# Kernel optimization log

Measured on AMD Instinct MI355X. Metric: run time of the kernel, lower is better.

## Reference

```python
import jax, jax.numpy as jnp
import numpy as np

V, E, L, H, B, T = 32000, 1024, 6, 16, 4, 1024
HS = E // H
FF = 4 * E


def setup_inputs() -> dict:
    key = jax.random.key(0)
    ks = jax.random.split(key, 16)
    s = 0.02
    n = lambda k, shp: jax.random.normal(k, shp, jnp.float32) * s
    return {
        "tokens": jax.random.randint(ks[0], (B, T), 0, V),
        "tok_emb": n(ks[1], (V, E)),
        "pos_emb": n(ks[2], (T, E)),
        "Wq": n(ks[3], (L, E, E)),
        "Wk": n(ks[4], (L, E, E)),
        "Wv": n(ks[5], (L, E, E)),
        "Wo": n(ks[6], (L, E, E)),
        "ln1_g": jnp.ones((L, E), jnp.float32),
        "ln1_b": jnp.zeros((L, E), jnp.float32),
        "W1": n(ks[7], (L, E, FF)),
        "b1": jnp.zeros((L, FF), jnp.float32),
        "W2": n(ks[8], (L, FF, E)),
        "b2": jnp.zeros((L, E), jnp.float32),
        "ln2_g": jnp.ones((L, E), jnp.float32),
        "ln2_b": jnp.zeros((L, E), jnp.float32),
        "lmh_w": n(ks[9], (E, V)),
        "lmh_b": jnp.zeros((V,), jnp.float32),
    }


def _layernorm(x, g, b):
    m = jnp.mean(x, axis=-1, keepdims=True)
    v = jnp.var(x, axis=-1, keepdims=True)
    return (x - m) * jax.lax.rsqrt(v + 1e-5) * g + b


def _forward(tokens, tok_emb, pos_emb, Wq, Wk, Wv, Wo, ln1_g, ln1_b,
             W1, b1, W2, b2, ln2_g, ln2_b, lmh_w, lmh_b):
    Bb, Tt = tokens.shape
    x = tok_emb[tokens] + pos_emb[:Tt]  # [B,T,E]
    mask = jnp.tril(jnp.ones((Tt, Tt), bool))  # causal
    scale = jnp.float32(E) ** -0.5  # NOTE: original scales by emb_dim, not head_size

    def block(x, p):
        wq, wk, wv, wo, g1, be1, w1, bb1, w2, bb2, g2, be2 = p
        h = _layernorm(x, g1, be1)
        q = (h @ wq).reshape(Bb, Tt, H, HS)
        k = (h @ wk).reshape(Bb, Tt, H, HS)
        v = (h @ wv).reshape(Bb, Tt, H, HS)
        scores = jnp.einsum('bqhd,bkhd->bhqk', q, k) * scale
        scores = jnp.where(mask, scores, -jnp.inf)
        w = jax.nn.softmax(scores, axis=-1)
        attn = jnp.einsum('bhqk,bkhd->bqhd', w, v).reshape(Bb, Tt, E)
        x = x + attn @ wo
        h2 = _layernorm(x, g2, be2)
        x = x + jax.nn.relu(h2 @ w1 + bb1) @ w2 + bb2
        return x, None

    x, _ = jax.lax.scan(block, x, (Wq, Wk, Wv, Wo, ln1_g, ln1_b,
                                   W1, b1, W2, b2, ln2_g, ln2_b))
    logits = x @ lmh_w + lmh_b  # [B,T,V]
    return logits


def reference(tokens, tok_emb, pos_emb, Wq, Wk, Wv, Wo, ln1_g, ln1_b,
              W1, b1, W2, b2, ln2_g, ln2_b, lmh_w, lmh_b):
    return _forward(tokens, tok_emb, pos_emb, Wq, Wk, Wv, Wo, ln1_g, ln1_b,
                    W1, b1, W2, b2, ln2_g, ln2_b, lmh_w, lmh_b)
```

## Files before the change

kernel.cpp:

```cpp
#include <hip/hip_runtime.h>
#include <cstdint>
#include <cstddef>

typedef __bf16 bf16;
typedef __attribute__((ext_vector_type(8))) __bf16 bf16x8;
typedef __attribute__((ext_vector_type(4))) float f32x4;

constexpr int kV = 32000, kE = 1024, kL = 6, kH = 16, kB = 4, kT = 1024;
constexpr int kHS = 64, kFF = 4096;
constexpr int kM = kB * kT;
constexpr float kScale = 0.03125f;

typedef __attribute__((address_space(1))) void gv_t;
typedef __attribute__((address_space(3))) void lv_t;

__device__ inline void gload_lds16(const void* g, void* l) {
  __builtin_amdgcn_global_load_lds((gv_t*)g, (lv_t*)l, 16, 0, 0);
}

enum { EPI_BF16 = 0, EPI_BF16_BIAS_RELU = 1, EPI_F32 = 2, EPI_F32_RES = 3, EPI_F32_BIAS = 4 };

template <int EPI>
__global__ __launch_bounds__(512, 2) void gemm256_k(
    const bf16* __restrict__ Ag, const bf16* __restrict__ Bg, void* Cg,
    const float* __restrict__ bias, const float* __restrict__ resid,
    int K, long lda, long ldb, long ldc) {
  extern __shared__ bf16 lds[];
  constexpr int SL = 8192;
  bf16* As = lds;
  bf16* Bs = lds + 4 * SL;

  const int tid = threadIdx.x, lane = tid & 63, w = tid >> 6;
  int bx = blockIdx.x, by = blockIdx.y;
  {
    int gx = gridDim.x, gy = gridDim.y;
    int nxy = gx * gy;
    int orig = by * gx + bx;
    int q = nxy >> 3, r = nxy & 7, xcd = orig & 7, idx = orig >> 3;
    int logical = (xcd < r ? xcd * (q + 1) : r * (q + 1) + (xcd - r) * q) + idx;
    bx = logical / gy;
    by = logical % gy;
  }
  const long tm = (long)by * 256, tn = (long)bx * 256;
  const int wr = w >> 2, wc = w & 3;
  const int lr = lane & 15, kg = lane >> 4;

  const int p0 = tid, p1 = 512 + tid;
  const int r0 = p0 >> 2, ls0 = (p0 & 3) ^ ((r0 >> 1) & 3);
  const int r1 = p1 >> 2, ls1 = (p1 & 3) ^ ((r1 >> 1) & 3);
  const bf16* a0 = Ag + (tm + r0) * lda + ls0 * 8;
  const bf16* a1 = Ag + (tm + r1) * lda + ls1 * 8;
  const bf16* b0 = Bg + (tn + r0) * ldb + ls0 * 8;
  const bf16* b1 = Bg + (tn + r1) * ldb + ls1 * 8;
  const int wb = w * 1024;

  auto stage = [&](int s) {
    const int slot = s & 3;
    const long k0 = (long)s * 32;
    char* Ab = (char*)As + slot * (SL * 2);
    char* Bb = (char*)Bs + slot * (SL * 2);
    gload_lds16(a0 + k0, Ab + wb);
    gload_lds16(a1 + k0, Ab + 8192 + wb);
    gload_lds16(b0 + k0, Bb + wb);
    gload_lds16(b1 + k0, Bb + 8192 + wb);
  };

  int aoff[8], boff[4];
#pragma unroll
  for (int mi = 0; mi < 8; mi++) {
    int ar = wr * 128 + mi * 16 + lr;
    aoff[mi] = ar * 64 + ((kg ^ ((ar >> 1) & 3)) << 4);
  }
#pragma unroll
  for (int ni = 0; ni < 4; ni++) {
    int br = wc * 64 + ni * 16 + lr;
    boff[ni] = br * 64 + ((kg ^ ((br >> 1) & 3)) << 4);
  }

  f32x4 acc[8][4] = {};
  stage(0);
  stage(1);
  stage(2);
  const int NS = K >> 5;
  for (int s = 0; s < NS; s++) {
    __builtin_amdgcn_sched_barrier(0);
    if (s <= NS - 3)
      asm volatile("s_waitcnt vmcnt(8)" ::: "memory");
    else if (s == NS - 2)
      asm volatile("s_waitcnt vmcnt(4)" ::: "memory");
    else
      asm volatile("s_waitcnt vmcnt(0)" ::: "memory");
    __builtin_amdgcn_s_barrier();
    __builtin_amdgcn_sched_barrier(0);
    if (s + 3 < NS) stage(s + 3);
    const char* Ab = (const char*)As + (s & 3) * (SL * 2);
    const char* Bb = (const char*)Bs + (s & 3) * (SL * 2);
    bf16x8 af[8], bfr[4];
#pragma unroll
    for (int mi = 0; mi < 8; mi++) af[mi] = *(const bf16x8*)(Ab + aoff[mi]);
#pragma unroll
    for (int ni = 0; ni < 4; ni++) bfr[ni] = *(const bf16x8*)(Bb + boff[ni]);
    __builtin_amdgcn_s_setprio(1);
#pragma unroll
    for (int mi = 0; mi < 8; mi++)
#pragma unroll
      for (int ni = 0; ni < 4; ni++)
        acc[mi][ni] =
            __builtin_amdgcn_mfma_f32_16x16x32_bf16(af[mi], bfr[ni], acc[mi][ni], 0, 0, 0);
    __builtin_amdgcn_s_setprio(0);
  }

#pragma unroll
  for (int mi = 0; mi < 8; mi++) {
#pragma unroll
    for (int ni = 0; ni < 4; ni++) {
      const long rr = tm + wr * 128 + mi * 16 + kg * 4;
      const long cc = tn + wc * 64 + ni * 16 + lr;
      float bi = 0.f;
      if constexpr (EPI == EPI_BF16_BIAS_RELU || EPI == EPI_F32_BIAS) bi = bias[cc];
      if constexpr (EPI == EPI_F32_RES) bi = bias ? bias[cc] : 0.f;
#pragma unroll
      for (int j = 0; j < 4; j++) {
        long off = (rr + j) * ldc + cc;
        float val = acc[mi][ni][j];
        if constexpr (EPI == EPI_BF16)
          ((bf16*)Cg)[off] = (bf16)val;
        else if constexpr (EPI == EPI_BF16_BIAS_RELU)
          ((bf16*)Cg)[off] = (bf16)fmaxf(val + bi, 0.f);
        else if constexpr (EPI == EPI_F32)
          ((float*)Cg)[off] = val;
        else if constexpr (EPI == EPI_F32_RES)
          ((float*)Cg)[off] = resid[off] + val + bi;
        else
          ((float*)Cg)[off] = val + bi;
      }
    }
  }
}

template <int BM, int BN, int WM, int WN, int EPI, bool CAUSAL>
__global__ __launch_bounds__((BM / WM) * (BN / WN) * 64) void gemm_k(
    const bf16* __restrict__ Ag, const bf16* __restrict__ Bg, void* Cg,
    const float* __restrict__ bias, const float* resid, int K, long lda, long ldb,
    long ldc, long sA1, long sA2, long sB1, long sB2, long sC1, long sC2, int zdiv) {
  constexpr int BK = 32;
  constexpr int NWM = BM / WM, NWN = BN / WN, NW = NWM * NWN, THREADS = NW * 64;
  constexpr int MI = WM / 16, NI = WN / 16;
  constexpr int A_CH = (BM * BK * 2) / (THREADS * 16);
  constexpr int B_CH = (BN * BK * 2) / (THREADS * 16);
  static_assert(A_CH >= 1 && B_CH >= 1, "staging chunks");
  __shared__ bf16 As[2][BM * BK];
  __shared__ bf16 Bs[2][BN * BK];
  const int tid = threadIdx.x, lane = tid & 63;
  int bx = blockIdx.x, by = blockIdx.y;
  const int z = blockIdx.z;
  if (gridDim.z == 1) {
    int gx = gridDim.x, gy = gridDim.y;
    int nxy = gx * gy;
    int orig = by * gx + bx;
    int q = nxy >> 3, r = nxy & 7, xcd = orig & 7, idx = orig >> 3;
    int logical = (xcd < r ? xcd * (q + 1) : r * (q + 1) + (xcd - r) * q) + idx;
    bx = logical / gy;
    by = logical % gy;
  }
  const long tm = (long)by * BM, tn = (long)bx * BN;
  if (CAUSAL && tn > tm + (BM - 1)) return;
  const int zq = z / zdiv, zr = z % zdiv;
  Ag += (long)zq * sA1 + (long)zr * sA2;
  Bg += (long)zq * sB1 + (long)zr * sB2;
  const long cbase = (long)zq * sC1 + (long)zr * sC2;
  const int w = tid >> 6;
  const int wr = w / NWN, wc = w % NWN;
  const int wm0 = wr * WM, wn0 = wc * WN;
  const int lr = lane & 15, kg = lane >> 4;
  f32x4 acc[MI][NI] = {};

  auto stage = [&](int buf, int k0) {
#pragma unroll
    for (int i = 0; i < A_CH; i++) {
      int qq = i * THREADS + tid;
      gload_lds16(Ag + (tm + (qq >> 2)) * lda + k0 + (qq & 3) * 8,
                  (char*)&As[buf][0] + (i * THREADS + (tid & ~63)) * 16);
    }
#pragma unroll
    for (int i = 0; i < B_CH; i++) {
      int qq = i * THREADS + tid;
      gload_lds16(Bg + (tn + (qq >> 2)) * ldb + k0 + (qq & 3) * 8,
                  (char*)&Bs[buf][0] + (i * THREADS + (tid & ~63)) * 16);
    }
  };

  const int nt = K / BK;
  stage(0, 0);
  __syncthreads();
  int cur = 0;
  for (int t = 0; t < nt; t++) {
    if (t + 1 < nt) stage(cur ^ 1, (t + 1) * BK);
    bf16x8 af[MI], bfr[NI];
#pragma unroll
    for (int mi = 0; mi < MI; mi++)
      af[mi] = *(const bf16x8*)&As[cur][(wm0 + mi * 16 + lr) * BK + kg * 8];
#pragma unroll
    for (int ni = 0; ni < NI; ni++)
      bfr[ni] = *(const bf16x8*)&Bs[cur][(wn0 + ni * 16 + lr) * BK + kg * 8];
#pragma unroll
    for (int mi = 0; mi < MI; mi++)
#pragma unroll
      for (int ni = 0; ni < NI; ni++)
        acc[mi][ni] =
            __builtin_amdgcn_mfma_f32_16x16x32_bf16(af[mi], bfr[ni], acc[mi][ni], 0, 0, 0);
    __syncthreads();
    cur ^= 1;
  }

#pragma unroll
  for (int mi = 0; mi < MI; mi++) {
#pragma unroll
    for (int ni = 0; ni < NI; ni++) {
      const long rr = tm + wm0 + mi * 16 + kg * 4;
      const long cc = tn + wn0 + ni * 16 + lr;
      float bi = 0.f;
      if constexpr (EPI == EPI_BF16_BIAS_RELU || EPI == EPI_F32_BIAS) bi = bias[cc];
      if constexpr (EPI == EPI_F32_RES) bi = bias ? bias[cc] : 0.f;
#pragma unroll
      for (int j = 0; j < 4; j++) {
        long off = cbase + (rr + j) * ldc + cc;
        float val = acc[mi][ni][j];
        if constexpr (EPI == EPI_BF16)
          ((bf16*)Cg)[off] = (bf16)val;
        else if constexpr (EPI == EPI_BF16_BIAS_RELU)
          ((bf16*)Cg)[off] = (bf16)fmaxf(val + bi, 0.f);
        else if constexpr (EPI == EPI_F32)
          ((float*)Cg)[off] = val;
        else if constexpr (EPI == EPI_F32_RES)
          ((float*)Cg)[off] = resid[off] + val + bi;
        else
          ((float*)Cg)[off] = val + bi;
      }
    }
  }
}

__global__ __launch_bounds__(256, 2) void fa_k(const bf16* __restrict__ qkv,
                                               bf16* __restrict__ out) {
  extern __shared__ bf16 lds[];
  char* L = (char*)lds;
  const int tid = threadIdx.x, lane = tid & 63, wq = tid >> 6;
  const int lr = lane & 15, kg = lane >> 4;
  const int bt = blockIdx.x, z = blockIdx.y;
  const int b = z >> 4, hh = z & 15;
  const long bq = (long)b * kT;
  const int q0 = bt * 128;
  const bf16* qbase = qkv + (bq + q0) * 3072 + hh * 64;

#pragma unroll
  for (int i = 0; i < 4; i++) {
    int p = i * 256 + tid;
    int row = p >> 3, s = p & 7;
    gload_lds16(qbase + (long)row * 3072 + ((s ^ (row & 7)) * 8),
                L + (i * 256 + (tid & ~63)) * 16);
  }
  auto stageKV = [&](int buf, int t) {
    const bf16* kb = qkv + (bq + t * 64) * 3072 + 1024 + hh * 64;
#pragma unroll
    for (int i = 0; i < 2; i++) {
      int p = i * 256 + tid;
      int key = p >> 3, s = p & 7;
      gload_lds16(kb + (long)key * 3072 + ((s ^ (key & 7)) * 8),
                  L + 16384 + buf * 8192 + (i * 256 + (tid & ~63)) * 16);
      gload_lds16(kb + (long)key * 3072 + 1024 + s * 8,
                  L + 32768 + buf * 8192 + (i * 256 + (tid & ~63)) * 16);
    }
  };
  stageKV(0, 0);
  __syncthreads();

  bf16x8 qf[2][2];
#pragma unroll
  for (int mi = 0; mi < 2; mi++)
#pragma unroll
    for (int ks = 0; ks < 2; ks++) {
      int qr = wq * 32 + mi * 16 + lr;
      qf[mi][ks] = *(const bf16x8*)(L + qr * 128 + ((ks * 64 + kg * 16) ^ ((qr & 7) << 4)));
    }

  f32x4 O[2][4] = {};
  float mrun[2][4], lrun[2][4];
#pragma unroll
  for (int mi = 0; mi < 2; mi++)
#pragma unroll
    for (int j = 0; j < 4; j++) {
      mrun[mi][j] = -3e38f;
      lrun[mi][j] = 0.f;
    }
  char* Pw = L + 58368 + wq * 4608;

  const int nt = 2 * bt + 2;
  int cur = 0;
  for (int t = 0; t < nt; t++) {
    if (t + 1 < nt) stageKV(cur ^ 1, t + 1);
    {
      const char* Vb = L + 32768 + cur * 8192;
      char* VTb = L + 49152;
#pragma unroll
      for (int i = 0; i < 2; i++) {
        int p = i * 256 + tid;
        int key = p >> 3, s = p & 7;
        bf16x8 vv = *(const bf16x8*)(Vb + p * 16);
#pragma unroll
        for (int e = 0; e < 8; e++)
          *(bf16*)(VTb + (s * 8 + e) * 144 + ((key * 2) ^ (s << 4))) = vv[e];
      }
    }
    asm volatile("s_waitcnt lgkmcnt(0)" ::: "memory");
    __builtin_amdgcn_sched_barrier(0);
    __builtin_amdgcn_s_barrier();
    __builtin_amdgcn_sched_barrier(0);

    const char* Kb = L + 16384 + cur * 8192;
    f32x4 S[2][4] = {};
#pragma unroll
    for (int ks = 0; ks < 2; ks++) {
      bf16x8 kf[4];
#pragma unroll
      for (int ni = 0; ni < 4; ni++) {
        int key = ni * 16 + lr;
        kf[ni] = *(const bf16x8*)(Kb + key * 128 + ((ks * 64 + kg * 16) ^ ((key & 7) << 4)));
      }
#pragma unroll
      for (int mi = 0; mi < 2; mi++)
#pragma unroll
        for (int ni = 0; ni < 4; ni++)
          S[mi][ni] = __builtin_amdgcn_mfma_f32_16x16x32_bf16(qf[mi][ks], kf[ni], S[mi][ni], 0, 0, 0);
    }

    const int kv0 = t * 64;
#pragma unroll
    for (int mi = 0; mi < 2; mi++) {
      const int qg = q0 + wq * 32 + mi * 16 + kg * 4;
#pragma unroll
      for (int j = 0; j < 4; j++) {
        float m0 = -3e38f;
#pragma unroll
        for (int ni = 0; ni < 4; ni++) {
          float v = (kv0 + ni * 16 + lr > qg + j) ? -3e38f : S[mi][ni][j];
          S[mi][ni][j] = v;
          m0 = fmaxf(m0, v);
        }
        m0 = fmaxf(m0, __shfl_xor(m0, 1));
        m0 = fmaxf(m0, __shfl_xor(m0, 2));
        m0 = fmaxf(m0, __shfl_xor(m0, 4));
        m0 = fmaxf(m0, __shfl_xor(m0, 8));
        float mnew = fmaxf(mrun[mi][j], m0);
        float alpha = __expf((mrun[mi][j] - mnew) * kScale);
        mrun[mi][j] = mnew;
        lrun[mi][j] *= alpha;
#pragma unroll
        for (int di = 0; di < 4; di++) O[mi][di][j] *= alpha;
        float rs = 0.f;
#pragma unroll
        for (int ni = 0; ni < 4; ni++) {
          float v = S[mi][ni][j];
          float p = (v <= -1e38f) ? 0.f : __expf((v - mnew) * kScale);
          S[mi][ni][j] = p;
          rs += p;
        }
        rs += __shfl_xor(rs, 1);
        rs += __shfl_xor(rs, 2);
        rs += __shfl_xor(rs, 4);
        rs += __shfl_xor(rs, 8);
        lrun[mi][j] += rs;
      }
#pragma unroll
      for (int ni = 0; ni < 4; ni++)
#pragma unroll
        for (int j = 0; j < 4; j++)
          *(bf16*)(Pw + (mi * 16 + kg * 4 + j) * 144 + (ni * 16 + lr) * 2) =
              (bf16)S[mi][ni][j];
    }
    asm volatile("s_waitcnt lgkmcnt(0)" ::: "memory");
    __builtin_amdgcn_sched_barrier(0);

    const char* VTb = L + 49152;
#pragma unroll
    for (int ks = 0; ks < 2; ks++) {
      bf16x8 pf[2], vf[4];
#pragma unroll
      for (int mi = 0; mi < 2; mi++)
        pf[mi] = *(const bf16x8*)(Pw + (mi * 16 + lr) * 144 + ks * 64 + kg * 16);
#pragma unroll
      for (int di = 0; di < 4; di++) {
        int d = di * 16 + lr;
        vf[di] = *(const bf16x8*)(VTb + d * 144 + ((ks * 64 + kg * 16) ^ (((d >> 3) & 7) << 4)));
      }
#pragma unroll
      for (int mi = 0; mi < 2; mi++)
#pragma unroll
        for (int di = 0; di < 4; di++)
          O[mi][di] = __builtin_amdgcn_mfma_f32_16x16x32_bf16(pf[mi], vf[di], O[mi][di], 0, 0, 0);
    }
    __syncthreads();
    cur ^= 1;
  }

#pragma unroll
  for (int mi = 0; mi < 2; mi++)
#pragma unroll
    for (int j = 0; j < 4; j++) {
      float inv = 1.f / lrun[mi][j];
      long grow = bq + q0 + wq * 32 + mi * 16 + kg * 4 + j;
#pragma unroll
      for (int di = 0; di < 4; di++)
        out[grow * kE + hh * 64 + di * 16 + lr] = (bf16)(O[mi][di][j] * inv);
    }
}

__global__ void tcvt_k(const float* __restrict__ in, bf16* __restrict__ out, int K, int N,
                       long in_zs, long out_zs) {
  __shared__ float t[32][33];
  long z = blockIdx.z;
  in += z * in_zs;
  out += z * out_zs;
  int n0 = blockIdx.x * 32, k0 = blockIdx.y * 32;
  int tx = threadIdx.x, ty = threadIdx.y;
#pragma unroll
  for (int i = 0; i < 32; i += 8) t[ty + i][tx] = in[(long)(k0 + ty + i) * N + n0 + tx];
  __syncthreads();
#pragma unroll
  for (int i = 0; i < 32; i += 8)
    out[(long)(n0 + ty + i) * K + k0 + tx] = (bf16)t[tx][ty + i];
}

__global__ void embed_k(const int* __restrict__ toks, const float* __restrict__ te,
                        const float* __restrict__ pe, float* __restrict__ x) {
  int row = blockIdx.x, tid = threadIdx.x;
  int t = row & (kT - 1);
  long tok = toks[row];
  float4 a = ((const float4*)(te + tok * kE))[tid];
  float4 p = ((const float4*)(pe + (long)t * kE))[tid];
  float4 r{a.x + p.x, a.y + p.y, a.z + p.z, a.w + p.w};
  ((float4*)(x + (long)row * kE))[tid] = r;
}

__global__ void ln_k(const float* __restrict__ x, const float* __restrict__ g,
                     const float* __restrict__ b, bf16* __restrict__ h) {
  int row = blockIdx.x, tid = threadIdx.x, lane = tid & 63, w = tid >> 6;
  const float4 v = ((const float4*)(x + (long)row * kE))[tid];
  float s = v.x + v.y + v.z + v.w;
  float ss = v.x * v.x + v.y * v.y + v.z * v.z + v.w * v.w;
#pragma unroll
  for (int o = 32; o; o >>= 1) {
    s += __shfl_xor(s, o);
    ss += __shfl_xor(ss, o);
  }
  __shared__ float r1[4], r2[4];
  if (lane == 0) { r1[w] = s; r2[w] = ss; }
  __syncthreads();
  s = r1[0] + r1[1] + r1[2] + r1[3];
  ss = r2[0] + r2[1] + r2[2] + r2[3];
  float mean = s * (1.f / kE);
  float var = ss * (1.f / kE) - mean * mean;
  float rs = rsqrtf(var + 1e-5f);
  float4 gg = ((const float4*)g)[tid];
  float4 bb = ((const float4*)b)[tid];
  union { bf16 o[4]; uint2 u; } pk;
  pk.o[0] = (bf16)((v.x - mean) * rs * gg.x + bb.x);
  pk.o[1] = (bf16)((v.y - mean) * rs * gg.y + bb.y);
  pk.o[2] = (bf16)((v.z - mean) * rs * gg.z + bb.z);
  pk.o[3] = (bf16)((v.w - mean) * rs * gg.w + bb.w);
  ((uint2*)(h + (long)row * kE))[tid] = pk.u;
}

__global__ void cast_k(const float* __restrict__ x, bf16* __restrict__ o) {
  long i = (long)blockIdx.x * 256 + threadIdx.x;
  float4 v = ((const float4*)x)[i];
  union { bf16 b[4]; uint2 u; } pk;
  pk.b[0] = (bf16)v.x;
  pk.b[1] = (bf16)v.y;
  pk.b[2] = (bf16)v.z;
  pk.b[3] = (bf16)v.w;
  ((uint2*)o)[i] = pk.u;
}

extern "C" void kernel_launch(void* const* d_in, const int* in_sizes, int n_in,
                              void* d_out, int out_size, void* d_ws, size_t ws_size,
                              hipStream_t stream) {
  const int* toks = (const int*)d_in[0];
  const float* te = (const float*)d_in[1];
  const float* pe = (const float*)d_in[2];
  const float* Wq = (const float*)d_in[3];
  const float* Wk = (const float*)d_in[4];
  const float* Wv = (const float*)d_in[5];
  const float* Wo = (const float*)d_in[6];
  const float* g1 = (const float*)d_in[7];
  const float* be1 = (const float*)d_in[8];
  const float* W1 = (const float*)d_in[9];
  const float* bb1 = (const float*)d_in[10];
  const float* W2 = (const float*)d_in[11];
  const float* bb2 = (const float*)d_in[12];
  const float* g2 = (const float*)d_in[13];
  const float* be2 = (const float*)d_in[14];
  const float* lmw = (const float*)d_in[15];
  const float* lmb = (const float*)d_in[16];

  hipFuncSetAttribute(reinterpret_cast<const void*>(&gemm256_k<EPI_BF16>),
                      hipFuncAttributeMaxDynamicSharedMemorySize, 131072);
  hipFuncSetAttribute(reinterpret_cast<const void*>(&gemm256_k<EPI_BF16_BIAS_RELU>),
                      hipFuncAttributeMaxDynamicSharedMemorySize, 131072);
  hipFuncSetAttribute(reinterpret_cast<const void*>(&gemm256_k<EPI_F32_BIAS>),
                      hipFuncAttributeMaxDynamicSharedMemorySize, 131072);
  hipFuncSetAttribute(reinterpret_cast<const void*>(&fa_k),
                      hipFuncAttributeMaxDynamicSharedMemorySize, 76800);

  char* ws = (char*)d_ws;
  size_t off = 0;
  auto alloc = [&](size_t bytes) -> char* {
    char* p = ws + off;
    off += (bytes + 255) & ~(size_t)255;
    return p;
  };
  bf16* WqkvT = (bf16*)alloc((size_t)kL * 3 * kE * kE * 2);
  bf16* WoT = (bf16*)alloc((size_t)kL * kE * kE * 2);
  bf16* W1T = (bf16*)alloc((size_t)kL * kE * kFF * 2);
  bf16* W2T = (bf16*)alloc((size_t)kL * kE * kFF * 2);
  bf16* lmT = (bf16*)alloc((size_t)kV * kE * 2);
  float* x = (float*)alloc((size_t)kM * kE * 4);
  bf16* h = (bf16*)alloc((size_t)kM * kE * 2);
  bf16* qkv = (bf16*)alloc((size_t)kM * 3 * kE * 2);
  bf16* at = (bf16*)alloc((size_t)kM * kE * 2);

  bf16* mid = (bf16*)d_out;

  const long EE = (long)kE * kE;
  dim3 tb(32, 8);
  tcvt_k<<<dim3(kE / 32, kE / 32, kL), tb, 0, stream>>>(Wq, WqkvT, kE, kE, EE, 3 * EE);
  tcvt_k<<<dim3(kE / 32, kE / 32, kL), tb, 0, stream>>>(Wk, WqkvT + EE, kE, kE, EE, 3 * EE);
  tcvt_k<<<dim3(kE / 32, kE / 32, kL), tb, 0, stream>>>(Wv, WqkvT + 2 * EE, kE, kE, EE, 3 * EE);
  tcvt_k<<<dim3(kE / 32, kE / 32, kL), tb, 0, stream>>>(Wo, WoT, kE, kE, EE, EE);
  tcvt_k<<<dim3(kFF / 32, kE / 32, kL), tb, 0, stream>>>(W1, W1T, kE, kFF, 4 * EE, 4 * EE);
  tcvt_k<<<dim3(kE / 32, kFF / 32, kL), tb, 0, stream>>>(W2, W2T, kFF, kE, 4 * EE, 4 * EE);
  tcvt_k<<<dim3(kV / 32, kE / 32, 1), tb, 0, stream>>>(lmw, lmT, kE, kV, 0, 0);

  embed_k<<<kM, 256, 0, stream>>>(toks, te, pe, x);

  for (int l = 0; l < kL; l++) {
    ln_k<<<kM, 256, 0, stream>>>(x, g1 + l * kE, be1 + l * kE, h);
    gemm256_k<EPI_BF16><<<dim3(3 * kE / 256, kM / 256), 512, 131072, stream>>>(
        h, WqkvT + (size_t)l * 3 * EE, qkv, nullptr, nullptr, kE, kE, kE, 3 * kE);
    fa_k<<<dim3(kT / 128, kB * kH), 256, 76800, stream>>>(qkv, at);
    gemm_k<128, 128, 64, 64, EPI_F32_RES, false><<<dim3(kE / 128, kM / 128, 1), 256, 0, stream>>>(
        at, WoT + (size_t)l * EE, x, nullptr, x, kE, kE, kE, kE, 0, 0, 0, 0, 0, 0, 1);
    ln_k<<<kM, 256, 0, stream>>>(x, g2 + l * kE, be2 + l * kE, h);
    gemm256_k<EPI_BF16_BIAS_RELU><<<dim3(kFF / 256, kM / 256), 512, 131072, stream>>>(
        h, W1T + (size_t)l * (size_t)kFF * kE, mid, bb1 + l * kFF, nullptr, kE, kE, kE, kFF);
    gemm_k<128, 128, 64, 64, EPI_F32_RES, false><<<dim3(kE / 128, kM / 128, 1), 256, 0, stream>>>(
        mid, W2T + (size_t)l * (size_t)kE * kFF, x, bb2 + l * kE, x, kFF, kFF, kFF, kE, 0, 0, 0,
        0, 0, 0, 1);
  }
  cast_k<<<kM * kE / 1024, 256, 0, stream>>>(x, h);
  gemm256_k<EPI_F32_BIAS><<<dim3(kV / 256, kM / 256), 512, 131072, stream>>>(
      h, lmT, d_out, lmb, nullptr, kE, kE, kE, kV);
}
```

Baseline: 2.428 ms.

## Restructure GEMM main loop into double-buffered 64-K ping-pong phases

Replaces the 4-slot, 32-K-per-stage software pipeline in the 256x256 GEMM with two 64KB buffers of 64-K tiles. Each tile is split into four quarter phases that interleave LDS fragment reads, staging of the next tile's quarter, and MFMA blocks, separated by workgroup barriers. The goal is finer overlap of global->LDS copies with MFMA and better hiding of LDS read latency. The cost is many more s_barriers per iteration and a shallower prefetch distance, which could stall waves. The attention kernel edits only swap inline asm for macros.

```diff
diff --git a/kernel.cpp b/kernel.cpp
--- a/kernel.cpp
+++ b/kernel.cpp
@@ -17,6 +17,11 @@
 __device__ inline void gload_lds16(const void* g, void* l) {
   __builtin_amdgcn_global_load_lds((gv_t*)g, (lv_t*)l, 16, 0, 0);
 }
+
+#define SB0() __builtin_amdgcn_sched_barrier(0)
+#define LGK0() asm volatile("s_waitcnt lgkmcnt(0)" ::: "memory")
+#define VM4() asm volatile("s_waitcnt vmcnt(4)" ::: "memory")
+#define VM0() asm volatile("s_waitcnt vmcnt(0)" ::: "memory")
 
 enum { EPI_BF16 = 0, EPI_BF16_BIAS_RELU = 1, EPI_F32 = 2, EPI_F32_RES = 3, EPI_F32_BIAS = 4 };
 
@@ -26,9 +31,7 @@
     const float* __restrict__ bias, const float* __restrict__ resid,
     int K, long lda, long ldb, long ldc) {
   extern __shared__ bf16 lds[];
-  constexpr int SL = 8192;
-  bf16* As = lds;
-  bf16* Bs = lds + 4 * SL;
+  char* Lb = (char*)lds;
 
   const int tid = threadIdx.x, lane = tid & 63, w = tid >> 6;
   int bx = blockIdx.x, by = blockIdx.y;
@@ -45,24 +48,20 @@
   const int wr = w >> 2, wc = w & 3;
   const int lr = lane & 15, kg = lane >> 4;
 
-  const int p0 = tid, p1 = 512 + tid;
-  const int r0 = p0 >> 2, ls0 = (p0 & 3) ^ ((r0 >> 1) & 3);
-  const int r1 = p1 >> 2, ls1 = (p1 & 3) ^ ((r1 >> 1) & 3);
-  const bf16* a0 = Ag + (tm + r0) * lda + ls0 * 8;
-  const bf16* a1 = Ag + (tm + r1) * lda + ls1 * 8;
-  const bf16* b0 = Bg + (tn + r0) * ldb + ls0 * 8;
-  const bf16* b1 = Bg + (tn + r1) * ldb + ls1 * 8;
-  const int wb = w * 1024;
-
-  auto stage = [&](int s) {
-    const int slot = s & 3;
-    const long k0 = (long)s * 32;
-    char* Ab = (char*)As + slot * (SL * 2);
-    char* Bb = (char*)Bs + slot * (SL * 2);
-    gload_lds16(a0 + k0, Ab + wb);
-    gload_lds16(a1 + k0, Ab + 8192 + wb);
-    gload_lds16(b0 + k0, Bb + wb);
-    gload_lds16(b1 + k0, Bb + 8192 + wb);
+  const int r0 = tid >> 2, g0 = (tid & 3) ^ ((r0 >> 1) & 3);
+  const int r1 = (512 + tid) >> 2, g1 = ((512 + tid) & 3) ^ ((r1 >> 1) & 3);
+  const bf16* a0 = Ag + (tm + r0) * lda + g0 * 8;
+  const bf16* a1 = Ag + (tm + r1) * lda + g1 * 8;
+  const bf16* b0 = Bg + (tn + r0) * ldb + g0 * 8;
+  const bf16* b1 = Bg + (tn + r1) * ldb + g1 * 8;
+  const int wdst = (tid & ~63) * 16;
+
+  auto stageH = [&](int buf, int which, long k0) {
+    char* dst = Lb + buf * 65536 + which * 16384;
+    const bf16* s0 = (which < 2) ? a0 : b0;
+    const bf16* s1 = (which < 2) ? a1 : b1;
+    gload_lds16(s0 + k0, dst + wdst);
+    gload_lds16(s1 + k0, dst + 8192 + wdst);
   };
 
   int aoff[8], boff[4];
@@ -78,36 +77,92 @@
   }
 
   f32x4 acc[8][4] = {};
-  stage(0);
-  stage(1);
-  stage(2);
-  const int NS = K >> 5;
-  for (int s = 0; s < NS; s++) {
-    __builtin_amdgcn_sched_barrier(0);
-    if (s <= NS - 3)
-      asm volatile("s_waitcnt vmcnt(8)" ::: "memory");
-    else if (s == NS - 2)
-      asm volatile("s_waitcnt vmcnt(4)" ::: "memory");
-    else
-      asm volatile("s_waitcnt vmcnt(0)" ::: "memory");
-    __builtin_amdgcn_s_barrier();
-    __builtin_amdgcn_sched_barrier(0);
-    if (s + 3 < NS) stage(s + 3);
-    const char* Ab = (const char*)As + (s & 3) * (SL * 2);
-    const char* Bb = (const char*)Bs + (s & 3) * (SL * 2);
-    bf16x8 af[8], bfr[4];
-#pragma unroll
-    for (int mi = 0; mi < 8; mi++) af[mi] = *(const bf16x8*)(Ab + aoff[mi]);
-#pragma unroll
-    for (int ni = 0; ni < 4; ni++) bfr[ni] = *(const bf16x8*)(Bb + boff[ni]);
+  stageH(0, 0, 0);
+  stageH(0, 2, 0);
+  stageH(0, 1, 32);
+  stageH(0, 3, 32);
+  VM4();
+  __syncthreads();
+
+  const int NT = K >> 6;
+  bf16x8 fa[4], fb[4], fa2[4];
+  for (int t = 0; t < NT; t++) {
+    const char* base = Lb + (t & 1) * 65536;
+    const int nb = (t + 1) & 1;
+    const bool pf = (t + 1 < NT);
+    const long kn = (long)(t + 1) * 64;
+#pragma unroll
+    for (int mi = 0; mi < 4; mi++) fa[mi] = *(const bf16x8*)(base + aoff[mi]);
+#pragma unroll
+    for (int ni = 0; ni < 4; ni++) fb[ni] = *(const bf16x8*)(base + 32768 + boff[ni]);
+    if (pf) stageH(nb, 0, kn);
+    SB0();
+    __builtin_amdgcn_s_barrier();
+    LGK0();
+    SB0();
     __builtin_amdgcn_s_setprio(1);
 #pragma unroll
-    for (int mi = 0; mi < 8; mi++)
+    for (int mi = 0; mi < 4; mi++)
 #pragma unroll
       for (int ni = 0; ni < 4; ni++)
-        acc[mi][ni] =
-            __builtin_amdgcn_mfma_f32_16x16x32_bf16(af[mi], bfr[ni], acc[mi][ni], 0, 0, 0);
+        acc[mi][ni] = __builtin_amdgcn_mfma_f32_16x16x32_bf16(fa[mi], fb[ni], acc[mi][ni], 0, 0, 0);
     __builtin_amdgcn_s_setprio(0);
+    SB0();
+    __builtin_amdgcn_s_barrier();
+#pragma unroll
+    for (int mi = 0; mi < 4; mi++) fa2[mi] = *(const bf16x8*)(base + aoff[4 + mi]);
+    if (pf) stageH(nb, 2, kn);
+    if (pf) VM4(); else VM0();
+    SB0();
+    __builtin_amdgcn_s_barrier();
+    LGK0();
+    SB0();
+    __builtin_amdgcn_s_setprio(1);
+#pragma unroll
+    for (int mi = 0; mi < 4; mi++)
+#pragma unroll
+      for (int ni = 0; ni < 4; ni++)
+        acc[4 + mi][ni] =
+            __builtin_amdgcn_mfma_f32_16x16x32_bf16(fa2[mi], fb[ni], acc[4 + mi][ni], 0, 0, 0);
+    __builtin_amdgcn_s_setprio(0);
+    SB0();
+    __builtin_amdgcn_s_barrier();
+#pragma unroll
+    for (int mi = 0; mi < 4; mi++) fa[mi] = *(const bf16x8*)(base + 16384 + aoff[mi]);
+#pragma unroll
+    for (int ni = 0; ni < 4; ni++) fb[ni] = *(const bf16x8*)(base + 49152 + boff[ni]);
+    if (pf) stageH(nb, 1, kn + 32);
+    SB0();
+    __builtin_amdgcn_s_barrier();
+    LGK0();
+    SB0();
+    __builtin_amdgcn_s_setprio(1);
+#pragma unroll
+    for (int mi = 0; mi < 4; mi++)
+#pragma unroll
+      for (int ni = 0; ni < 4; ni++)
+        acc[mi][ni] = __builtin_amdgcn_mfma_f32_16x16x32_bf16(fa[mi], fb[ni], acc[mi][ni], 0, 0, 0);
+    __builtin_amdgcn_s_setprio(0);
+    SB0();
+    __builtin_amdgcn_s_barrier();
+#pragma unroll
+    for (int mi = 0; mi < 4; mi++) fa2[mi] = *(const bf16x8*)(base + 16384 + aoff[4 + mi]);
+    if (pf) stageH(nb, 3, kn + 32);
+    if (pf) VM4();
+    SB0();
+    __builtin_amdgcn_s_barrier();
+    LGK0();
+    SB0();
+    __builtin_amdgcn_s_setprio(1);
+#pragma unroll
+    for (int mi = 0; mi < 4; mi++)
+#pragma unroll
+      for (int ni = 0; ni < 4; ni++)
+        acc[4 + mi][ni] =
+            __builtin_amdgcn_mfma_f32_16x16x32_bf16(fa2[mi], fb[ni], acc[4 + mi][ni], 0, 0, 0);
+    __builtin_amdgcn_s_setprio(0);
+    SB0();
+    __builtin_amdgcn_s_barrier();
   }
 
 #pragma unroll
@@ -312,10 +367,10 @@
           *(bf16*)(VTb + (s * 8 + e) * 144 + ((key * 2) ^ (s << 4))) = vv[e];
       }
     }
-    asm volatile("s_waitcnt lgkmcnt(0)" ::: "memory");
-    __builtin_amdgcn_sched_barrier(0);
-    __builtin_amdgcn_s_barrier();
-    __builtin_amdgcn_sched_barrier(0);
+    LGK0();
+    SB0();
+    __builtin_amdgcn_s_barrier();
+    SB0();
 
     const char* Kb = L + 16384 + cur * 8192;
     f32x4 S[2][4] = {};
@@ -378,8 +433,8 @@
           *(bf16*)(Pw + (mi * 16 + kg * 4 + j) * 144 + (ni * 16 + lr) * 2) =
               (bf16)S[mi][ni][j];
     }
-    asm volatile("s_waitcnt lgkmcnt(0)" ::: "memory");
-    __builtin_amdgcn_sched_barrier(0);
+    LGK0();
+    SB0();
 
     const char* VTb = L + 49152;
 #pragma unroll
```

After: 2.436 ms. About the same (+0.3%).

## Pair causal attention query tiles per block and use ring-buffered 128-tile W2 GEMM

Applied to the files above, without the earlier changes.

The flash-attention kernel now processes two query tiles per block (tile p and 7-p), so every block does the same amount of causal work and the grid shrinks to four blocks per head. The FFN down-projection GEMM moves to a new 128x128 kernel with a 4-slot global_load_lds ring buffer and deeper prefetch, replacing the 2-buffer generic GEMM. Both changes aim to reduce tail imbalance and memory-latency stalls. In exchange, the attention launch has fewer blocks, and the new GEMM uses 64KB of LDS, which may limit occupancy.

```diff
diff --git a/kernel.cpp b/kernel.cpp
--- a/kernel.cpp
+++ b/kernel.cpp
@@ -18,7 +18,20 @@
   __builtin_amdgcn_global_load_lds((gv_t*)g, (lv_t*)l, 16, 0, 0);
 }
 
+#define SB0() __builtin_amdgcn_sched_barrier(0)
+#define LGK0() asm volatile("s_waitcnt lgkmcnt(0)" ::: "memory")
+
 enum { EPI_BF16 = 0, EPI_BF16_BIAS_RELU = 1, EPI_F32 = 2, EPI_F32_RES = 3, EPI_F32_BIAS = 4 };
+
+__device__ inline void xcd_swz(int& bx, int& by) {
+  int gx = gridDim.x, gy = gridDim.y;
+  int nxy = gx * gy;
+  int orig = by * gx + bx;
+  int q = nxy >> 3, r = nxy & 7, xcd = orig & 7, idx = orig >> 3;
+  int logical = (xcd < r ? xcd * (q + 1) : r * (q + 1) + (xcd - r) * q) + idx;
+  bx = logical / gy;
+  by = logical % gy;
+}
 
 template <int EPI>
 __global__ __launch_bounds__(512, 2) void gemm256_k(
@@ -32,15 +45,7 @@
 
   const int tid = threadIdx.x, lane = tid & 63, w = tid >> 6;
   int bx = blockIdx.x, by = blockIdx.y;
-  {
-    int gx = gridDim.x, gy = gridDim.y;
-    int nxy = gx * gy;
-    int orig = by * gx + bx;
-    int q = nxy >> 3, r = nxy & 7, xcd = orig & 7, idx = orig >> 3;
-    int logical = (xcd < r ? xcd * (q + 1) : r * (q + 1) + (xcd - r) * q) + idx;
-    bx = logical / gy;
-    by = logical % gy;
-  }
+  xcd_swz(bx, by);
   const long tm = (long)by * 256, tn = (long)bx * 256;
   const int wr = w >> 2, wc = w & 3;
   const int lr = lane & 15, kg = lane >> 4;
@@ -83,7 +88,7 @@
   stage(2);
   const int NS = K >> 5;
   for (int s = 0; s < NS; s++) {
-    __builtin_amdgcn_sched_barrier(0);
+    SB0();
     if (s <= NS - 3)
       asm volatile("s_waitcnt vmcnt(8)" ::: "memory");
     else if (s == NS - 2)
@@ -91,7 +96,7 @@
     else
       asm volatile("s_waitcnt vmcnt(0)" ::: "memory");
     __builtin_amdgcn_s_barrier();
-    __builtin_amdgcn_sched_barrier(0);
+    SB0();
     if (s + 3 < NS) stage(s + 3);
     const char* Ab = (const char*)As + (s & 3) * (SL * 2);
     const char* Bb = (const char*)Bs + (s & 3) * (SL * 2);
@@ -115,6 +120,112 @@
 #pragma unroll
     for (int ni = 0; ni < 4; ni++) {
       const long rr = tm + wr * 128 + mi * 16 + kg * 4;
+      const long cc = tn + wc * 64 + ni * 16 + lr;
+      float bi = 0.f;
+      if constexpr (EPI == EPI_BF16_BIAS_RELU || EPI == EPI_F32_BIAS) bi = bias[cc];
+      if constexpr (EPI == EPI_F32_RES) bi = bias ? bias[cc] : 0.f;
+#pragma unroll
+      for (int j = 0; j < 4; j++) {
+        long off = (rr + j) * ldc + cc;
+        float val = acc[mi][ni][j];
+        if constexpr (EPI == EPI_BF16)
+          ((bf16*)Cg)[off] = (bf16)val;
+        else if constexpr (EPI == EPI_BF16_BIAS_RELU)
+          ((bf16*)Cg)[off] = (bf16)fmaxf(val + bi, 0.f);
+        else if constexpr (EPI == EPI_F32)
+          ((float*)Cg)[off] = val;
+        else if constexpr (EPI == EPI_F32_RES)
+          ((float*)Cg)[off] = resid[off] + val + bi;
+        else
+          ((float*)Cg)[off] = val + bi;
+      }
+    }
+  }
+}
+
+template <int EPI>
+__global__ __launch_bounds__(256, 2) void ring128_k(
+    const bf16* __restrict__ Ag, const bf16* __restrict__ Bg, void* Cg,
+    const float* __restrict__ bias, const float* __restrict__ resid,
+    int K, long lda, long ldb, long ldc) {
+  extern __shared__ bf16 lds[];
+  char* Lb = (char*)lds;
+  const int tid = threadIdx.x, lane = tid & 63, w = tid >> 6;
+  int bx = blockIdx.x, by = blockIdx.y;
+  xcd_swz(bx, by);
+  const long tm = (long)by * 128, tn = (long)bx * 128;
+  const int wr = w >> 1, wc = w & 1;
+  const int lr = lane & 15, kg = lane >> 4;
+
+  const int r0 = tid >> 2, g0 = (tid & 3) ^ ((r0 >> 1) & 3);
+  const int r1 = (256 + tid) >> 2, g1 = ((256 + tid) & 3) ^ ((r1 >> 1) & 3);
+  const bf16* a0 = Ag + (tm + r0) * lda + g0 * 8;
+  const bf16* a1 = Ag + (tm + r1) * lda + g1 * 8;
+  const bf16* b0 = Bg + (tn + r0) * ldb + g0 * 8;
+  const bf16* b1 = Bg + (tn + r1) * ldb + g1 * 8;
+  const int wb = w * 1024;
+
+  auto stage = [&](int s) {
+    const int slot = s & 3;
+    const long k0 = (long)s * 32;
+    char* Ab = Lb + slot * 16384;
+    char* Bb = Ab + 8192;
+    gload_lds16(a0 + k0, Ab + wb);
+    gload_lds16(a1 + k0, Ab + 4096 + wb);
+    gload_lds16(b0 + k0, Bb + wb);
+    gload_lds16(b1 + k0, Bb + 4096 + wb);
+  };
+
+  int aoff[4], boff[4];
+#pragma unroll
+  for (int mi = 0; mi < 4; mi++) {
+    int ar = wr * 64 + mi * 16 + lr;
+    aoff[mi] = ar * 64 + ((kg ^ ((ar >> 1) & 3)) << 4);
+  }
+#pragma unroll
+  for (int ni = 0; ni < 4; ni++) {
+    int br = wc * 64 + ni * 16 + lr;
+    boff[ni] = br * 64 + ((kg ^ ((br >> 1) & 3)) << 4);
+  }
+
+  f32x4 acc[4][4] = {};
+  stage(0);
+  stage(1);
+  stage(2);
+  const int NS = K >> 5;
+  for (int s = 0; s < NS; s++) {
+    SB0();
+    if (s <= NS - 3)
+      asm volatile("s_waitcnt vmcnt(8)" ::: "memory");
+    else if (s == NS - 2)
+      asm volatile("s_waitcnt vmcnt(4)" ::: "memory");
+    else
+      asm volatile("s_waitcnt vmcnt(0)" ::: "memory");
+    __builtin_amdgcn_s_barrier();
+    SB0();
+    if (s + 3 < NS) stage(s + 3);
+    const char* Ab = Lb + (s & 3) * 16384;
+    const char* Bb = Ab + 8192;
+    bf16x8 af[4], bfr[4];
+#pragma unroll
+    for (int mi = 0; mi < 4; mi++) af[mi] = *(const bf16x8*)(Ab + aoff[mi]);
+#pragma unroll
+    for (int ni = 0; ni < 4; ni++) bfr[ni] = *(const bf16x8*)(Bb + boff[ni]);
+    __builtin_amdgcn_s_setprio(1);
+#pragma unroll
+    for (int mi = 0; mi < 4; mi++)
+#pragma unroll
+      for (int ni = 0; ni < 4; ni++)
+        acc[mi][ni] =
+            __builtin_amdgcn_mfma_f32_16x16x32_bf16(af[mi], bfr[ni], acc[mi][ni], 0, 0, 0);
+    __builtin_amdgcn_s_setprio(0);
+  }
+
+#pragma unroll
+  for (int mi = 0; mi < 4; mi++) {
+#pragma unroll
+    for (int ni = 0; ni < 4; ni++) {
+      const long rr = tm + wr * 64 + mi * 16 + kg * 4;
       const long cc = tn + wc * 64 + ni * 16 + lr;
       float bi = 0.f;
       if constexpr (EPI == EPI_BF16_BIAS_RELU || EPI == EPI_F32_BIAS) bi = bias[cc];
@@ -154,15 +265,7 @@
   const int tid = threadIdx.x, lane = tid & 63;
   int bx = blockIdx.x, by = blockIdx.y;
   const int z = blockIdx.z;
-  if (gridDim.z == 1) {
-    int gx = gridDim.x, gy = gridDim.y;
-    int nxy = gx * gy;
-    int orig = by * gx + bx;
-    int q = nxy >> 3, r = nxy & 7, xcd = orig & 7, idx = orig >> 3;
-    int logical = (xcd < r ? xcd * (q + 1) : r * (q + 1) + (xcd - r) * q) + idx;
-    bx = logical / gy;
-    by = logical % gy;
-  }
+  if (gridDim.z == 1) xcd_swz(bx, by);
   const long tm = (long)by * BM, tn = (long)bx * BN;
   if (CAUSAL && tn > tm + (BM - 1)) return;
   const int zq = z / zdiv, zr = z % zdiv;
@@ -247,19 +350,10 @@
   char* L = (char*)lds;
   const int tid = threadIdx.x, lane = tid & 63, wq = tid >> 6;
   const int lr = lane & 15, kg = lane >> 4;
-  const int bt = blockIdx.x, z = blockIdx.y;
+  const int pair = blockIdx.x, z = blockIdx.y;
   const int b = z >> 4, hh = z & 15;
   const long bq = (long)b * kT;
-  const int q0 = bt * 128;
-  const bf16* qbase = qkv + (bq + q0) * 3072 + hh * 64;
-
-#pragma unroll
-  for (int i = 0; i < 4; i++) {
-    int p = i * 256 + tid;
-    int row = p >> 3, s = p & 7;
-    gload_lds16(qbase + (long)row * 3072 + ((s ^ (row & 7)) * 8),
-                L + (i * 256 + (tid & ~63)) * 16);
-  }
+
   auto stageKV = [&](int buf, int t) {
     const bf16* kb = qkv + (bq + t * 64) * 3072 + 1024 + hh * 64;
 #pragma unroll
@@ -272,147 +366,164 @@
                   L + 32768 + buf * 8192 + (i * 256 + (tid & ~63)) * 16);
     }
   };
-  stageKV(0, 0);
-  __syncthreads();
-
-  bf16x8 qf[2][2];
-#pragma unroll
-  for (int mi = 0; mi < 2; mi++)
-#pragma unroll
-    for (int ks = 0; ks < 2; ks++) {
-      int qr = wq * 32 + mi * 16 + lr;
-      qf[mi][ks] = *(const bf16x8*)(L + qr * 128 + ((ks * 64 + kg * 16) ^ ((qr & 7) << 4)));
-    }
-
-  f32x4 O[2][4] = {};
-  float mrun[2][4], lrun[2][4];
-#pragma unroll
-  for (int mi = 0; mi < 2; mi++)
-#pragma unroll
-    for (int j = 0; j < 4; j++) {
-      mrun[mi][j] = -3e38f;
-      lrun[mi][j] = 0.f;
-    }
   char* Pw = L + 58368 + wq * 4608;
 
-  const int nt = 2 * bt + 2;
-  int cur = 0;
-  for (int t = 0; t < nt; t++) {
-    if (t + 1 < nt) stageKV(cur ^ 1, t + 1);
-    {
-      const char* Vb = L + 32768 + cur * 8192;
-      char* VTb = L + 49152;
-#pragma unroll
-      for (int i = 0; i < 2; i++) {
-        int p = i * 256 + tid;
-        int key = p >> 3, s = p & 7;
-        bf16x8 vv = *(const bf16x8*)(Vb + p * 16);
-#pragma unroll
-        for (int e = 0; e < 8; e++)
-          *(bf16*)(VTb + (s * 8 + e) * 144 + ((key * 2) ^ (s << 4))) = vv[e];
-      }
-    }
-    asm volatile("s_waitcnt lgkmcnt(0)" ::: "memory");
-    __builtin_amdgcn_sched_barrier(0);
-    __builtin_amdgcn_s_barrier();
-    __builtin_amdgcn_sched_barrier(0);
-
-    const char* Kb = L + 16384 + cur * 8192;
-    f32x4 S[2][4] = {};
-#pragma unroll
-    for (int ks = 0; ks < 2; ks++) {
-      bf16x8 kf[4];
-#pragma unroll
-      for (int ni = 0; ni < 4; ni++) {
-        int key = ni * 16 + lr;
-        kf[ni] = *(const bf16x8*)(Kb + key * 128 + ((ks * 64 + kg * 16) ^ ((key & 7) << 4)));
-      }
-#pragma unroll
-      for (int mi = 0; mi < 2; mi++)
+  for (int sidx = 0; sidx < 2; sidx++) {
+    const int qt = sidx ? 7 - pair : pair;
+    const int q0 = qt * 128;
+    const bf16* qbase = qkv + (bq + q0) * 3072 + hh * 64;
+
+#pragma unroll
+    for (int i = 0; i < 4; i++) {
+      int p = i * 256 + tid;
+      int row = p >> 3, s = p & 7;
+      gload_lds16(qbase + (long)row * 3072 + ((s ^ (row & 7)) * 8),
+                  L + (i * 256 + (tid & ~63)) * 16);
+    }
+    stageKV(0, 0);
+    __syncthreads();
+
+    bf16x8 qf[2][2];
+#pragma unroll
+    for (int mi = 0; mi < 2; mi++)
+#pragma unroll
+      for (int ks = 0; ks < 2; ks++) {
+        int qr = wq * 32 + mi * 16 + lr;
+        qf[mi][ks] = *(const bf16x8*)(L + qr * 128 + ((ks * 64 + kg * 16) ^ ((qr & 7) << 4)));
+      }
+
+    f32x4 O[2][4] = {};
+    float mrun[2][4], lrun[2][4];
+#pragma unroll
+    for (int mi = 0; mi < 2; mi++)
+#pragma unroll
+      for (int j = 0; j < 4; j++) {
+        mrun[mi][j] = -3e38f;
+        lrun[mi][j] = 0.f;
+      }
+
+    const int nt = 2 * qt + 2;
+    int cur = 0;
+    for (int t = 0; t < nt; t++) {
+      if (t + 1 < nt) stageKV(cur ^ 1, t + 1);
+      {
+        const char* Vb = L + 32768 + cur * 8192;
+        char* VTb = L + 49152;
+#pragma unroll
+        for (int i = 0; i < 2; i++) {
+          int p = i * 256 + tid;
+          int key = p >> 3, s = p & 7;
+          bf16x8 vv = *(const bf16x8*)(Vb + p * 16);
+#pragma unroll
+          for (int e = 0; e < 8; e++)
+            *(bf16*)(VTb + (s * 8 + e) * 144 + ((key * 2) ^ (s << 4))) = vv[e];
+        }
+      }
+      LGK0();
+      SB0();
+      __builtin_amdgcn_s_barrier();
+      SB0();
+
+      const char* Kb = L + 16384 + cur * 8192;
+      f32x4 S[2][4] = {};
+#pragma unroll
+      for (int ks = 0; ks < 2; ks++) {
+        bf16x8 kf[4];
+#pragma unroll
+        for (int ni = 0; ni < 4; ni++) {
+          int key = ni * 16 + lr;
+          kf[ni] = *(const bf16x8*)(Kb + key * 128 + ((ks * 64 + kg * 16) ^ ((key & 7) << 4)));
+        }
+#pragma unroll
+        for (int mi = 0; mi < 2; mi++)
+#pragma unroll
+          for (int ni = 0; ni < 4; ni++)
+            S[mi][ni] =
+                __builtin_amdgcn_mfma_f32_16x16x32_bf16(qf[mi][ks], kf[ni], S[mi][ni], 0, 0, 0);
+      }
+
+      const int kv0 = t * 64;
+#pragma unroll
+      for (int mi = 0; mi < 2; mi++) {
+        const int qg = q0 + wq * 32 + mi * 16 + kg * 4;
+#pragma unroll
+        for (int j = 0; j < 4; j++) {
+          float m0 = -3e38f;
+#pragma unroll
+          for (int ni = 0; ni < 4; ni++) {
+            float v = (kv0 + ni * 16 + lr > qg + j) ? -3e38f : S[mi][ni][j];
+            S[mi][ni][j] = v;
+            m0 = fmaxf(m0, v);
+          }
+          m0 = fmaxf(m0, __shfl_xor(m0, 1));
+          m0 = fmaxf(m0, __shfl_xor(m0, 2));
+          m0 = fmaxf(m0, __shfl_xor(m0, 4));
+          m0 = fmaxf(m0, __shfl_xor(m0, 8));
+          float mnew = fmaxf(mrun[mi][j], m0);
+          float alpha = __expf((mrun[mi][j] - mnew) * kScale);
+          mrun[mi][j] = mnew;
+          lrun[mi][j] *= alpha;
+#pragma unroll
+          for (int di = 0; di < 4; di++) O[mi][di][j] *= alpha;
+          float rs = 0.f;
+#pragma unroll
+          for (int ni = 0; ni < 4; ni++) {
+            float v = S[mi][ni][j];
+            float p = (v <= -1e38f) ? 0.f : __expf((v - mnew) * kScale);
+            S[mi][ni][j] = p;
+            rs += p;
+          }
+          rs += __shfl_xor(rs, 1);
+          rs += __shfl_xor(rs, 2);
+          rs += __shfl_xor(rs, 4);
+          rs += __shfl_xor(rs, 8);
+          lrun[mi][j] += rs;
+        }
 #pragma unroll
         for (int ni = 0; ni < 4; ni++)
-          S[mi][ni] = __builtin_amdgcn_mfma_f32_16x16x32_bf16(qf[mi][ks], kf[ni], S[mi][ni], 0, 0, 0);
-    }
-
-    const int kv0 = t * 64;
-#pragma unroll
-    for (int mi = 0; mi < 2; mi++) {
-      const int qg = q0 + wq * 32 + mi * 16 + kg * 4;
+#pragma unroll
+          for (int j = 0; j < 4; j++)
+            *(bf16*)(Pw + (mi * 16 + kg * 4 + j) * 144 + (ni * 16 + lr) * 2) =
+                (bf16)S[mi][ni][j];
+      }
+      LGK0();
+      SB0();
+
+      const char* VTb = L + 49152;
+#pragma unroll
+      for (int ks = 0; ks < 2; ks++) {
+        bf16x8 pf[2], vf[4];
+#pragma unroll
+        for (int mi = 0; mi < 2; mi++)
+          pf[mi] = *(const bf16x8*)(Pw + (mi * 16 + lr) * 144 + ks * 64 + kg * 16);
+#pragma unroll
+        for (int di = 0; di < 4; di++) {
+          int d = di * 16 + lr;
+          vf[di] =
+              *(const bf16x8*)(VTb + d * 144 + ((ks * 64 + kg * 16) ^ (((d >> 3) & 7) << 4)));
+        }
+#pragma unroll
+        for (int mi = 0; mi < 2; mi++)
+#pragma unroll
+          for (int di = 0; di < 4; di++)
+            O[mi][di] =
+                __builtin_amdgcn_mfma_f32_16x16x32_bf16(pf[mi], vf[di], O[mi][di], 0, 0, 0);
+      }
+      __syncthreads();
+      cur ^= 1;
+    }
+
+#pragma unroll
+    for (int mi = 0; mi < 2; mi++)
 #pragma unroll
       for (int j = 0; j < 4; j++) {
-        float m0 = -3e38f;
-#pragma unroll
-        for (int ni = 0; ni < 4; ni++) {
-          float v = (kv0 + ni * 16 + lr > qg + j) ? -3e38f : S[mi][ni][j];
-          S[mi][ni][j] = v;
-          m0 = fmaxf(m0, v);
-        }
-        m0 = fmaxf(m0, __shfl_xor(m0, 1));
-        m0 = fmaxf(m0, __shfl_xor(m0, 2));
-        m0 = fmaxf(m0, __shfl_xor(m0, 4));
-        m0 = fmaxf(m0, __shfl_xor(m0, 8));
-        float mnew = fmaxf(mrun[mi][j], m0);
-        float alpha = __expf((mrun[mi][j] - mnew) * kScale);
-        mrun[mi][j] = mnew;
-        lrun[mi][j] *= alpha;
-#pragma unroll
-        for (int di = 0; di < 4; di++) O[mi][di][j] *= alpha;
-        float rs = 0.f;
-#pragma unroll
-        for (int ni = 0; ni < 4; ni++) {
-          float v = S[mi][ni][j];
-          float p = (v <= -1e38f) ? 0.f : __expf((v - mnew) * kScale);
-          S[mi][ni][j] = p;
-          rs += p;
-        }
-        rs += __shfl_xor(rs, 1);
-        rs += __shfl_xor(rs, 2);
-        rs += __shfl_xor(rs, 4);
-        rs += __shfl_xor(rs, 8);
-        lrun[mi][j] += rs;
-      }
-#pragma unroll
-      for (int ni = 0; ni < 4; ni++)
-#pragma unroll
-        for (int j = 0; j < 4; j++)
-          *(bf16*)(Pw + (mi * 16 + kg * 4 + j) * 144 + (ni * 16 + lr) * 2) =
-              (bf16)S[mi][ni][j];
-    }
-    asm volatile("s_waitcnt lgkmcnt(0)" ::: "memory");
-    __builtin_amdgcn_sched_barrier(0);
-
-    const char* VTb = L + 49152;
-#pragma unroll
-    for (int ks = 0; ks < 2; ks++) {
-      bf16x8 pf[2], vf[4];
-#pragma unroll
-      for (int mi = 0; mi < 2; mi++)
-        pf[mi] = *(const bf16x8*)(Pw + (mi * 16 + lr) * 144 + ks * 64 + kg * 16);
-#pragma unroll
-      for (int di = 0; di < 4; di++) {
-        int d = di * 16 + lr;
-        vf[di] = *(const bf16x8*)(VTb + d * 144 + ((ks * 64 + kg * 16) ^ (((d >> 3) & 7) << 4)));
-      }
-#pragma unroll
-      for (int mi = 0; mi < 2; mi++)
+        float inv = 1.f / lrun[mi][j];
+        long grow = bq + q0 + wq * 32 + mi * 16 + kg * 4 + j;
 #pragma unroll
         for (int di = 0; di < 4; di++)
-          O[mi][di] = __builtin_amdgcn_mfma_f32_16x16x32_bf16(pf[mi], vf[di], O[mi][di], 0, 0, 0);
-    }
-    __syncthreads();
-    cur ^= 1;
-  }
-
-#pragma unroll
-  for (int mi = 0; mi < 2; mi++)
-#pragma unroll
-    for (int j = 0; j < 4; j++) {
-      float inv = 1.f / lrun[mi][j];
-      long grow = bq + q0 + wq * 32 + mi * 16 + kg * 4 + j;
-#pragma unroll
-      for (int di = 0; di < 4; di++)
-        out[grow * kE + hh * 64 + di * 16 + lr] = (bf16)(O[mi][di][j] * inv);
-    }
+          out[grow * kE + hh * 64 + di * 16 + lr] = (bf16)(O[mi][di][j] * inv);
+      }
+  }
 }
 
 __global__ void tcvt_k(const float* __restrict__ in, bf16* __restrict__ out, int K, int N,
@@ -509,6 +620,8 @@
                       hipFuncAttributeMaxDynamicSharedMemorySize, 131072);
   hipFuncSetAttribute(reinterpret_cast<const void*>(&gemm256_k<EPI_F32_BIAS>),
                       hipFuncAttributeMaxDynamicSharedMemorySize, 131072);
+  hipFuncSetAttribute(reinterpret_cast<const void*>(&ring128_k<EPI_F32_RES>),
+                      hipFuncAttributeMaxDynamicSharedMemorySize, 65536);
   hipFuncSetAttribute(reinterpret_cast<const void*>(&fa_k),
                       hipFuncAttributeMaxDynamicSharedMemorySize, 76800);
 
@@ -547,15 +660,14 @@
     ln_k<<<kM, 256, 0, stream>>>(x, g1 + l * kE, be1 + l * kE, h);
     gemm256_k<EPI_BF16><<<dim3(3 * kE / 256, kM / 256), 512, 131072, stream>>>(
         h, WqkvT + (size_t)l * 3 * EE, qkv, nullptr, nullptr, kE, kE, kE, 3 * kE);
-    fa_k<<<dim3(kT / 128, kB * kH), 256, 76800, stream>>>(qkv, at);
+    fa_k<<<dim3(4, kB * kH), 256, 76800, stream>>>(qkv, at);
     gemm_k<128, 128, 64, 64, EPI_F32_RES, false><<<dim3(kE / 128, kM / 128, 1), 256, 0, stream>>>(
         at, WoT + (size_t)l * EE, x, nullptr, x, kE, kE, kE, kE, 0, 0, 0, 0, 0, 0, 1);
     ln_k<<<kM, 256, 0, stream>>>(x, g2 + l * kE, be2 + l * kE, h);
     gemm256_k<EPI_BF16_BIAS_RELU><<<dim3(kFF / 256, kM / 256), 512, 131072, stream>>>(
         h, W1T + (size_t)l * (size_t)kFF * kE, mid, bb1 + l * kFF, nullptr, kE, kE, kE, kFF);
-    gemm_k<128, 128, 64, 64, EPI_F32_RES, false><<<dim3(kE / 128, kM / 128, 1), 256, 0, stream>>>(
-        mid, W2T + (size_t)l * (size_t)kE * kFF, x, bb2 + l * kE, x, kFF, kFF, kFF, kE, 0, 0, 0,
-        0, 0, 0, 1);
+    ring128_k<EPI_F32_RES><<<dim3(kE / 128, kM / 128), 256, 65536, stream>>>(
+        mid, W2T + (size_t)l * (size_t)kE * kFF, x, bb2 + l * kE, x, kFF, kFF, kFF, kE);
   }
   cast_k<<<kM * kE / 1024, 256, 0, stream>>>(x, h);
   gemm256_k<EPI_F32_BIAS><<<dim3(kV / 256, kM / 256), 512, 131072, stream>>>(
```

Measured after the change: 2.122 ms. 12.6% less time.
